# Kernel optimization log

Measured on AMD Instinct MI355X. Metric: run time of the kernel, lower is better.

Reference implementation:

```python
import jax, jax.numpy as jnp
import numpy as np

B, L, D = 4, 64, 512          # batch, trajectory length, d_model
DI, N, DC, R = 1024, 16, 4, 32  # d_inner, d_state, d_conv, dt_rank
NL = 4                         # n_layers
SD, AD, MEL = 17, 6, 1000      # state_dim, act_dim, max_ep_len
EPS = 1e-5


def setup_inputs() -> dict:
    key = jax.random.key(0)
    ks = iter(jax.random.split(key, 40))
    nrm = lambda shp, s=0.02: jax.random.normal(next(ks), shp, jnp.float32) * s
    inp = {
        "states": jax.random.normal(next(ks), (B, L, SD), jnp.float32),
        "actions": jax.random.normal(next(ks), (B, L, AD), jnp.float32),
        "returns_to_go": jax.random.normal(next(ks), (B, L, 1), jnp.float32),
        "constraints_to_go": jax.random.normal(next(ks), (B, L, 1), jnp.float32),
        "timesteps": jax.random.randint(next(ks), (B, L), 0, MEL, jnp.int32),
        # embedding / projection heads (torch Linear: y = x @ W.T + b)
        "es_w": nrm((D, SD)), "es_b": jnp.zeros((D,), jnp.float32),
        "ea_w": nrm((D, AD)), "ea_b": jnp.zeros((D,), jnp.float32),
        "er_w": nrm((D, 1)), "er_b": jnp.zeros((D,), jnp.float32),
        "ec_w": nrm((D, 1)), "ec_b": jnp.zeros((D,), jnp.float32),
        "et_w": nrm((MEL, D)),
        # per-layer Mamba params, stacked on leading NL axis
        "ln_w": jnp.ones((NL, D), jnp.float32), "ln_b": jnp.zeros((NL, D), jnp.float32),
        "in_w": nrm((NL, 2 * DI, D)),
        "conv_w": nrm((NL, DI, DC), 0.1), "conv_b": jnp.zeros((NL, DI), jnp.float32),
        "xp_w": nrm((NL, R + 2 * N, DI)),
        "dtp_w": nrm((NL, DI, R), 0.1),
        "dtp_b": jnp.full((NL, DI), -4.6, jnp.float32) + nrm((NL, DI), 0.1),
        "A_log": jnp.broadcast_to(jnp.log(jnp.arange(1, N + 1, dtype=jnp.float32)), (NL, DI, N)) * jnp.ones((NL, DI, 1), jnp.float32),
        "Dp": jnp.ones((NL, DI), jnp.float32),
        "out_w": nrm((NL, D, DI)),
        # final norm + heads
        "fn_w": jnp.ones((D,), jnp.float32), "fn_b": jnp.zeros((D,), jnp.float32),
        "ps_w": nrm((SD, D)), "ps_b": jnp.zeros((SD,), jnp.float32),
        "pa_w": nrm((AD, D)), "pa_b": jnp.zeros((AD,), jnp.float32),
    }
    return inp


def layernorm(x, w, b):
    mu = jnp.mean(x, -1, keepdims=True)
    var = jnp.mean(jnp.square(x - mu), -1, keepdims=True)
    return (x - mu) * jax.lax.rsqrt(var + EPS) * w + b


def selective_scan(u, delta, A, Bm, Cm, Dp):
    # u, delta: (B,T,DI); A: (DI,N); Bm, Cm: (B,T,N); Dp: (DI,)
    dA = jnp.exp(delta[..., None] * A)                      # (B,T,DI,N)
    dBu = delta[..., None] * Bm[:, :, None, :] * u[..., None]

    def step(h, xs):
        dA_t, dBu_t, C_t = xs
        h = dA_t * h + dBu_t                                # (B,DI,N)
        y = jnp.einsum('bdn,bn->bd', h, C_t)
        return h, y

    h0 = jnp.zeros((u.shape[0], u.shape[2], A.shape[1]), u.dtype)
    xs = (dA.transpose(1, 0, 2, 3), dBu.transpose(1, 0, 2, 3), Cm.transpose(1, 0, 2))
    _, ys = jax.lax.scan(step, h0, xs)
    return ys.transpose(1, 0, 2) + u * Dp


def mamba_mixer(x, in_w, conv_w, conv_b, xp_w, dtp_w, dtp_b, A_log, Dp, out_w):
    T = x.shape[1]
    xz = x @ in_w.T                                         # (B,T,2*DI)
    xm, z = jnp.split(xz, 2, axis=-1)
    # causal depthwise conv1d, kernel DC
    xpad = jnp.pad(xm, ((0, 0), (DC - 1, 0), (0, 0)))
    xc = sum(xpad[:, k:k + T, :] * conv_w[:, k] for k in range(DC)) + conv_b
    xc = jax.nn.silu(xc)
    dbc = xc @ xp_w.T                                       # (B,T,R+2N)
    dt, Bm, Cm = jnp.split(dbc, [R, R + N], axis=-1)
    delta = jax.nn.softplus(dt @ dtp_w.T + dtp_b)           # (B,T,DI)
    y = selective_scan(xc, delta, -jnp.exp(A_log), Bm, Cm, Dp)
    y = y * jax.nn.silu(z)
    return y @ out_w.T


def reference(states, actions, returns_to_go, constraints_to_go, timesteps,
              es_w, es_b, ea_w, ea_b, er_w, er_b, ec_w, ec_b, et_w,
              ln_w, ln_b, in_w, conv_w, conv_b, xp_w, dtp_w, dtp_b, A_log, Dp, out_w,
              fn_w, fn_b, ps_w, ps_b, pa_w, pa_b):
    te = et_w[timesteps]                                    # (B,L,D)
    se = states @ es_w.T + es_b + te
    ae = actions @ ea_w.T + ea_b + te
    re = returns_to_go @ er_w.T + er_b + te
    ce = constraints_to_go @ ec_w.T + ec_b + te
    # interleave (r, c, s, a) per timestep -> (B, 4L, D)
    x = jnp.stack((re, ce, se, ae), axis=2).reshape(B, 4 * L, D)
    for i in range(NL):
        x = x + mamba_mixer(layernorm(x, ln_w[i], ln_b[i]),
                            in_w[i], conv_w[i], conv_b[i], xp_w[i],
                            dtp_w[i], dtp_b[i], A_log[i], Dp[i], out_w[i])
    x = layernorm(x, fn_w, fn_b)
    outputs = x.reshape(B, L, 4, D).transpose(0, 2, 1, 3)   # (B,4,L,D)
    state_preds = outputs[:, 3] @ ps_w.T + ps_b             # from action tokens
    action_preds = outputs[:, 2] @ pa_w.T + pa_b            # from state tokens
    return state_preds, action_preds
```

## Files before the change

### kernel.cpp

```cpp
#include <hip/hip_runtime.h>
#include <math.h>

#define B_ 4
#define L_ 64
#define D_ 512
#define DI_ 1024
#define N_ 16
#define DC_ 4
#define R_ 32
#define NL_ 4
#define SD_ 17
#define AD_ 6
#define T_ 256
#define CH3_ 32
#define TC3_ 8
#define DL3_ 8

#define NW_IN  (NL_ * 2 * DI_ * D_)
#define NW_OUT (NL_ * D_ * DI_)
#define NW_XP  (NL_ * 64 * DI_)
#define NW_TOT (NW_IN + NW_OUT + NW_XP)

typedef short bf16x8 __attribute__((ext_vector_type(8)));
typedef float f32x4 __attribute__((ext_vector_type(4)));

__device__ __forceinline__ float silu_f(float v) { return v / (1.f + __expf(-v)); }
__device__ __forceinline__ float softplus_f(float v) {
    return fmaxf(v, 0.f) + log1pf(__expf(-fabsf(v)));
}
__device__ __forceinline__ unsigned short f2bs(float f) {
    unsigned u = __float_as_uint(f);
    u += 0x7fffu + ((u >> 16) & 1u);
    return (unsigned short)(u >> 16);
}
__device__ __forceinline__ float bs2f(unsigned short s) {
    return __uint_as_float(((unsigned)s) << 16);
}

__global__ __launch_bounds__(256) void wcvt_kernel(
    const float* __restrict__ in_w, const float* __restrict__ out_w,
    const float* __restrict__ xp_w, unsigned short* __restrict__ wb)
{
    const int i = blockIdx.x * 256 + threadIdx.x;
    if (i >= NW_TOT / 4) return;
    const int e = i * 4;
    const float* src; int off;
    if (e < NW_IN)               { src = in_w;  off = e; }
    else if (e < NW_IN + NW_OUT) { src = out_w; off = e - NW_IN; }
    else                         { src = xp_w;  off = e - NW_IN - NW_OUT; }
    const float4 v = *(const float4*)(src + off);
    ushort4 o;
    o.x = f2bs(v.x); o.y = f2bs(v.y); o.z = f2bs(v.z); o.w = f2bs(v.w);
    *(ushort4*)(wb + e) = o;
}

__global__ __launch_bounds__(512) void embed_kernel(
    const float* __restrict__ states, const float* __restrict__ actions,
    const float* __restrict__ rtg, const float* __restrict__ ctg,
    const int* __restrict__ ts,
    const float* __restrict__ es_w, const float* __restrict__ es_b,
    const float* __restrict__ ea_w, const float* __restrict__ ea_b,
    const float* __restrict__ er_w, const float* __restrict__ er_b,
    const float* __restrict__ ec_w, const float* __restrict__ ec_b,
    const float* __restrict__ et_w, float* __restrict__ x)
{
    const int bl = blockIdx.x;
    const int d = threadIdx.x;
    const float te = et_w[(size_t)ts[bl] * D_ + d];
    const float r = rtg[bl] * er_w[d] + er_b[d] + te;
    const float c = ctg[bl] * ec_w[d] + ec_b[d] + te;
    float s = es_b[d] + te;
#pragma unroll
    for (int k = 0; k < SD_; ++k) s += states[bl * SD_ + k] * es_w[d * SD_ + k];
    float a = ea_b[d] + te;
#pragma unroll
    for (int k = 0; k < AD_; ++k) a += actions[bl * AD_ + k] * ea_w[d * AD_ + k];
    float* xp = x + (size_t)bl * 4 * D_;
    xp[0 * D_ + d] = r;
    xp[1 * D_ + d] = c;
    xp[2 * D_ + d] = s;
    xp[3 * D_ + d] = a;
}

template <int MODE>
__global__ __launch_bounds__(256) void ln2_kernel(
    float* __restrict__ x, const float* __restrict__ p0,
    const float* __restrict__ p1,
    const float* __restrict__ w, const float* __restrict__ b,
    void* __restrict__ o_)
{
    const int tok = blockIdx.x;
    const int tid = threadIdx.x;
    float2 v = reinterpret_cast<float2*>(x + (size_t)tok * D_)[tid];
    if (MODE >= 1) {
        const float2 a0 = reinterpret_cast<const float2*>(p0 + (size_t)tok * D_)[tid];
        const float2 a1 = reinterpret_cast<const float2*>(p1 + (size_t)tok * D_)[tid];
        v.x += a0.x + a1.x;
        v.y += a0.y + a1.y;
        reinterpret_cast<float2*>(x + (size_t)tok * D_)[tid] = v;
    }
    float s = v.x + v.y;
#pragma unroll
    for (int off = 1; off < 64; off <<= 1) s += __shfl_xor(s, off);
    __shared__ float red[8];
    const int wv = tid >> 6;
    if ((tid & 63) == 0) red[wv] = s;
    __syncthreads();
    const float mean = (red[0] + red[1] + red[2] + red[3]) * (1.f / D_);
    const float dx = v.x - mean, dy = v.y - mean;
    float q = dx * dx + dy * dy;
#pragma unroll
    for (int off = 1; off < 64; off <<= 1) q += __shfl_xor(q, off);
    if ((tid & 63) == 0) red[4 + wv] = q;
    __syncthreads();
    const float var = (red[4] + red[5] + red[6] + red[7]) * (1.f / D_);
    const float r = rsqrtf(var + 1e-5f);
    const int d0 = tid * 2;
    const float o0 = dx * r * w[d0] + b[d0];
    const float o1 = dy * r * w[d0 + 1] + b[d0 + 1];
    if (MODE == 2) {
        float* o = (float*)o_;
        o[(size_t)tok * D_ + d0] = o0;
        o[(size_t)tok * D_ + d0 + 1] = o1;
    } else {
        unsigned short* o = (unsigned short*)o_;
        o[(size_t)tok * D_ + d0] = f2bs(o0);
        o[(size_t)tok * D_ + d0 + 1] = f2bs(o1);
    }
}

template <int MR, int NR, int EPI, int KT>
__global__ __launch_bounds__(256) void gemm3(
    const unsigned short* __restrict__ A, int lda,
    const unsigned short* __restrict__ W, int ldw,
    float* __restrict__ C, unsigned short* __restrict__ Cb1,
    unsigned short* __restrict__ Cb2, int N)
{
    const int lane = threadIdx.x & 63, wid = threadIdx.x >> 6;
    const int r = lane & 15, kq = lane >> 4;
    const int wm = blockIdx.y * (2 * MR * 16) + (wid >> 1) * (MR * 16);
    const int wn = blockIdx.x * (2 * NR * 16) + (wid & 1) * (NR * 16);
    const int kb = (EPI == 4) ? blockIdx.z * KT : 0;
    f32x4 acc[MR][NR] = {};
#pragma unroll 4
    for (int k0 = 0; k0 < KT; k0 += 32) {
        bf16x8 a[MR], b[NR];
#pragma unroll
        for (int i = 0; i < MR; ++i)
            a[i] = *(const bf16x8*)(A + (size_t)(wm + i * 16 + r) * lda + kb + k0 + kq * 8);
#pragma unroll
        for (int j = 0; j < NR; ++j)
            b[j] = *(const bf16x8*)(W + (size_t)(wn + j * 16 + r) * ldw + kb + k0 + kq * 8);
#pragma unroll
        for (int i = 0; i < MR; ++i)
#pragma unroll
            for (int j = 0; j < NR; ++j)
                acc[i][j] = __builtin_amdgcn_mfma_f32_16x16x32_bf16(a[i], b[j], acc[i][j], 0, 0, 0);
    }
#pragma unroll
    for (int i = 0; i < MR; ++i)
#pragma unroll
        for (int j = 0; j < NR; ++j)
#pragma unroll
            for (int g = 0; g < 4; ++g) {
                const int row = wm + i * 16 + kq * 4 + g;
                const int col = wn + j * 16 + r;
                const float val = acc[i][j][g];
                if (EPI == 3) {
                    if (col < DI_) Cb1[(size_t)row * DI_ + col] = f2bs(val);
                    else Cb2[(size_t)row * DI_ + (col - DI_)] = f2bs(silu_f(val));
                } else if (EPI == 4) {
                    C[(size_t)blockIdx.z * (1024 * 512) + (size_t)row * 512 + col] = val;
                } else {
                    C[(size_t)row * N + col] = val;
                }
            }
}

__global__ __launch_bounds__(256) void convxp_kernel(
    const unsigned short* __restrict__ xmb, const float* __restrict__ cw,
    const float* __restrict__ cb, const unsigned short* __restrict__ Wb,
    unsigned short* __restrict__ xcb, float* __restrict__ dbc)
{
    __shared__ unsigned short sA[16 * 1024];
    __shared__ float red[4][16][64];
    const int tid = threadIdx.x;
    const int m0 = blockIdx.x * 16;
    for (int task = tid; task < 16 * 128; task += 256) {
        const int rr = task >> 7;
        const int dd0 = (task & 127) * 8;
        const int row = m0 + rr;
        const int t = row & (T_ - 1);
        float4 cw4[8];
#pragma unroll
        for (int j = 0; j < 8; ++j) cw4[j] = ((const float4*)cw)[dd0 + j];
        float acc[8];
#pragma unroll
        for (int j = 0; j < 8; ++j) acc[j] = cb[dd0 + j];
#pragma unroll
        for (int k = 0; k < DC_; ++k) {
            if (t - 3 + k >= 0) {
                const bf16x8 v = *(const bf16x8*)(xmb + (size_t)(row - 3 + k) * DI_ + dd0);
#pragma unroll
                for (int j = 0; j < 8; ++j) {
                    const float wk = (k == 0) ? cw4[j].x : (k == 1) ? cw4[j].y
                                   : (k == 2) ? cw4[j].z : cw4[j].w;
                    acc[j] += wk * bs2f((unsigned short)v[j]);
                }
            }
        }
        bf16x8 ov;
#pragma unroll
        for (int j = 0; j < 8; ++j) ov[j] = (short)f2bs(silu_f(acc[j]));
        *(bf16x8*)(xcb + (size_t)row * DI_ + dd0) = ov;
        const int byteoff = (rr * 2048 + dd0 * 2) ^ ((rr & 7) << 4);
        *(bf16x8*)((char*)sA + byteoff) = ov;
    }
    __syncthreads();
    const int wid = tid >> 6, lane = tid & 63;
    const int r = lane & 15, kq = lane >> 4;
    f32x4 acc4[4] = {};
    const int k00 = wid * 256;
#pragma unroll
    for (int ks = 0; ks < 8; ++ks) {
        const int k0 = k00 + ks * 32;
        const int abyte = (r * 2048 + (k0 + kq * 8) * 2) ^ ((r & 7) << 4);
        const bf16x8 a = *(const bf16x8*)((const char*)sA + abyte);
#pragma unroll
        for (int j = 0; j < 4; ++j) {
            const bf16x8 bfr = *(const bf16x8*)(Wb + (size_t)(j * 16 + r) * DI_ + k0 + kq * 8);
            acc4[j] = __builtin_amdgcn_mfma_f32_16x16x32_bf16(a, bfr, acc4[j], 0, 0, 0);
        }
    }
#pragma unroll
    for (int j = 0; j < 4; ++j)
#pragma unroll
        for (int g = 0; g < 4; ++g)
            red[wid][kq * 4 + g][j * 16 + r] = acc4[j][g];
    __syncthreads();
    for (int i = tid; i < 1024; i += 256) {
        const int row = i >> 6, col = i & 63;
        const float s = red[0][row][col] + red[1][row][col] +
                        red[2][row][col] + red[3][row][col];
        dbc[(size_t)(m0 + row) * 64 + col] = s;
    }
}

__global__ __launch_bounds__(256, 3) void scan_kernel(
    const unsigned short* __restrict__ xcb, const float* __restrict__ dbc,
    const float* __restrict__ dtw, const float* __restrict__ dtbias,
    const float* __restrict__ A_log, const float* __restrict__ Dp,
    const unsigned short* __restrict__ zs, unsigned short* __restrict__ ygb)
{
    __shared__ float dlt_s[T_][DL3_ + 1];
    __shared__ float Sl[CH3_][DL3_][17];
    __shared__ float Pl[CH3_][DL3_][17];
    const int tid = threadIdx.x;
    const int dl = tid & (DL3_ - 1);
    const int c = tid >> 3;
    const int b = blockIdx.x >> 7;
    const int d = (blockIdx.x & 127) * DL3_ + dl;
    const int row0 = b * T_ + c * TC3_;
    {
        const float4* Wp = (const float4*)(dtw + (size_t)d * R_);
        float4 w4[8];
#pragma unroll
        for (int q = 0; q < 8; ++q) w4[q] = Wp[q];
        const float bias = dtbias[d];
#pragma unroll
        for (int t = 0; t < TC3_; ++t) {
            const float4* Ap = (const float4*)(dbc + (size_t)(row0 + t) * 64);
            float acc = bias;
#pragma unroll
            for (int q = 0; q < 8; ++q) {
                const float4 a4 = Ap[q];
                acc += a4.x * w4[q].x + a4.y * w4[q].y + a4.z * w4[q].z + a4.w * w4[q].w;
            }
            dlt_s[c * TC3_ + t][dl] = softplus_f(acc);
        }
    }
    float Av[N_];
    {
        const float4* Alp = (const float4*)(A_log + (size_t)d * N_);
#pragma unroll
        for (int q = 0; q < 4; ++q) {
            const float4 v = Alp[q];
            Av[q * 4 + 0] = -__expf(v.x);
            Av[q * 4 + 1] = -__expf(v.y);
            Av[q * 4 + 2] = -__expf(v.z);
            Av[q * 4 + 3] = -__expf(v.w);
        }
    }
    __syncthreads();
    const unsigned short* up = xcb + (size_t)row0 * DI_ + d;
    const float* bc = dbc + (size_t)row0 * 64;
    float h[N_];
#pragma unroll
    for (int n = 0; n < N_; ++n) h[n] = 0.f;
    float dsum = 0.f;
#pragma unroll
    for (int t = 0; t < TC3_; ++t) {
        const float dt_t = dlt_s[c * TC3_ + t][dl];
        dsum += dt_t;
        const float dbu = dt_t * bs2f(up[t * DI_]);
#pragma unroll
        for (int q = 0; q < 4; ++q) {
            const float4 b4 = *(const float4*)(bc + t * 64 + R_ + q * 4);
            h[q * 4 + 0] = __expf(dt_t * Av[q * 4 + 0]) * h[q * 4 + 0] + dbu * b4.x;
            h[q * 4 + 1] = __expf(dt_t * Av[q * 4 + 1]) * h[q * 4 + 1] + dbu * b4.y;
            h[q * 4 + 2] = __expf(dt_t * Av[q * 4 + 2]) * h[q * 4 + 2] + dbu * b4.z;
            h[q * 4 + 3] = __expf(dt_t * Av[q * 4 + 3]) * h[q * 4 + 3] + dbu * b4.w;
        }
    }
#pragma unroll
    for (int n = 0; n < N_; ++n) {
        Sl[c][dl][n] = h[n];
        Pl[c][dl][n] = __expf(Av[n] * dsum);
    }
    __syncthreads();
    if (tid < DL3_ * N_) {
        const int dd = tid >> 4, nn = tid & 15;
        float hin = 0.f;
#pragma unroll
        for (int c2 = 0; c2 < CH3_; ++c2) {
            const float t2 = Pl[c2][dd][nn] * hin + Sl[c2][dd][nn];
            Sl[c2][dd][nn] = hin;
            hin = t2;
        }
    }
    __syncthreads();
#pragma unroll
    for (int n = 0; n < N_; ++n) h[n] = Sl[c][dl][n];
    const float Dd = Dp[d];
    const unsigned short* zp = zs + (size_t)row0 * DI_ + d;
    unsigned short* yp = ygb + (size_t)row0 * DI_ + d;
#pragma unroll
    for (int t = 0; t < TC3_; ++t) {
        const float dt_t = dlt_s[c * TC3_ + t][dl];
        const float ut = bs2f(up[t * DI_]);
        const float dbu = dt_t * ut;
        float y = ut * Dd;
#pragma unroll
        for (int q = 0; q < 4; ++q) {
            const float4 b4 = *(const float4*)(bc + t * 64 + R_ + q * 4);
            const float4 c4 = *(const float4*)(bc + t * 64 + R_ + N_ + q * 4);
            h[q * 4 + 0] = __expf(dt_t * Av[q * 4 + 0]) * h[q * 4 + 0] + dbu * b4.x;
            h[q * 4 + 1] = __expf(dt_t * Av[q * 4 + 1]) * h[q * 4 + 1] + dbu * b4.y;
            h[q * 4 + 2] = __expf(dt_t * Av[q * 4 + 2]) * h[q * 4 + 2] + dbu * b4.z;
            h[q * 4 + 3] = __expf(dt_t * Av[q * 4 + 3]) * h[q * 4 + 3] + dbu * b4.w;
            y += h[q * 4 + 0] * c4.x + h[q * 4 + 1] * c4.y
               + h[q * 4 + 2] * c4.z + h[q * 4 + 3] * c4.w;
        }
        yp[t * DI_] = f2bs(y * bs2f(zp[t * DI_]));
    }
}

__global__ __launch_bounds__(256) void heads_kernel(
    const float* __restrict__ xn,
    const float* __restrict__ ps_w, const float* __restrict__ ps_b,
    const float* __restrict__ pa_w, const float* __restrict__ pa_b,
    float* __restrict__ out)
{
    const int idx = blockIdx.x * 4 + (threadIdx.x >> 6);
    const int lane = threadIdx.x & 63;
    const int bl = idx / 23, j = idx % 23;
    const float* tok;
    const float* wrow;
    float bias;
    float* dst;
    if (j < SD_) {
        tok = xn + ((size_t)bl * 4 + 3) * D_;
        wrow = ps_w + (size_t)j * D_;
        bias = ps_b[j];
        dst = out + (size_t)bl * SD_ + j;
    } else {
        const int jj = j - SD_;
        tok = xn + ((size_t)bl * 4 + 2) * D_;
        wrow = pa_w + (size_t)jj * D_;
        bias = pa_b[jj];
        dst = out + (size_t)B_ * L_ * SD_ + (size_t)bl * AD_ + jj;
    }
    float s = 0.f;
    for (int dd = lane; dd < D_; dd += 64) s += tok[dd] * wrow[dd];
#pragma unroll
    for (int off = 1; off < 64; off <<= 1) s += __shfl_xor(s, off);
    if (lane == 0) *dst = s + bias;
}

extern "C" void kernel_launch(void* const* d_in, const int* in_sizes, int n_in,
                              void* d_out, int out_size, void* d_ws, size_t ws_size,
                              hipStream_t stream)
{
    const float* states  = (const float*)d_in[0];
    const float* actions = (const float*)d_in[1];
    const float* rtg     = (const float*)d_in[2];
    const float* ctg     = (const float*)d_in[3];
    const int*   ts      = (const int*)d_in[4];
    const float* es_w = (const float*)d_in[5];  const float* es_b = (const float*)d_in[6];
    const float* ea_w = (const float*)d_in[7];  const float* ea_b = (const float*)d_in[8];
    const float* er_w = (const float*)d_in[9];  const float* er_b = (const float*)d_in[10];
    const float* ec_w = (const float*)d_in[11]; const float* ec_b = (const float*)d_in[12];
    const float* et_w = (const float*)d_in[13];
    const float* ln_w = (const float*)d_in[14]; const float* ln_b = (const float*)d_in[15];
    const float* in_w = (const float*)d_in[16];
    const float* conv_w = (const float*)d_in[17]; const float* conv_b = (const float*)d_in[18];
    const float* xp_w = (const float*)d_in[19];
    const float* dtp_w = (const float*)d_in[20]; const float* dtp_b = (const float*)d_in[21];
    const float* A_log = (const float*)d_in[22]; const float* Dp = (const float*)d_in[23];
    const float* out_w = (const float*)d_in[24];
    const float* fn_w = (const float*)d_in[25]; const float* fn_b = (const float*)d_in[26];
    const float* ps_w = (const float*)d_in[27]; const float* ps_b = (const float*)d_in[28];
    const float* pa_w = (const float*)d_in[29]; const float* pa_b = (const float*)d_in[30];
    float* out = (float*)d_out;

    float* ws   = (float*)d_ws;
    float* x    = ws;
    float* xn   = x + 524288;
    float* p    = xn + 524288;
    float* dbc  = p + 1048576;
    unsigned short* xnb = (unsigned short*)(dbc + 65536);
    unsigned short* xmb = xnb + 524288;
    unsigned short* xcb = xmb + 1048576;
    unsigned short* zs  = xcb + 1048576;
    unsigned short* ygb = zs + 1048576;
    unsigned short* wb  = ygb + 1048576;
    unsigned short* wb_in  = wb;
    unsigned short* wb_out = wb + NW_IN;
    unsigned short* wb_xp  = wb + NW_IN + NW_OUT;

    wcvt_kernel<<<(NW_TOT / 4 + 255) / 256, 256, 0, stream>>>(in_w, out_w, xp_w, wb);
    embed_kernel<<<B_ * L_, D_, 0, stream>>>(states, actions, rtg, ctg, ts,
        es_w, es_b, ea_w, ea_b, er_w, er_b, ec_w, ec_b, et_w, x);

    for (int i = 0; i < NL_; ++i) {
        if (i == 0)
            ln2_kernel<0><<<B_ * T_, 256, 0, stream>>>(
                x, nullptr, nullptr, ln_w, ln_b, xnb);
        else
            ln2_kernel<1><<<B_ * T_, 256, 0, stream>>>(
                x, p, p + 524288, ln_w + i * D_, ln_b + i * D_, xnb);
        gemm3<2, 2, 3, 512><<<dim3(32, 16), 256, 0, stream>>>(
            xnb, D_, wb_in + (size_t)i * 2 * DI_ * D_, D_, nullptr, xmb, zs, 2 * DI_);
        convxp_kernel<<<64, 256, 0, stream>>>(
            xmb, conv_w + i * DI_ * DC_, conv_b + i * DI_,
            wb_xp + (size_t)i * 64 * DI_, xcb, dbc);
        scan_kernel<<<B_ * (DI_ / DL3_), 256, 0, stream>>>(
            xcb, dbc, dtp_w + (size_t)i * DI_ * R_, dtp_b + i * DI_,
            A_log + (size_t)i * DI_ * N_, Dp + i * DI_, zs, ygb);
        gemm3<2, 2, 4, 512><<<dim3(8, 16, 2), 256, 0, stream>>>(
            ygb, DI_, wb_out + (size_t)i * D_ * DI_, DI_, p, nullptr, nullptr, D_);
    }

    ln2_kernel<2><<<B_ * T_, 256, 0, stream>>>(x, p, p + 524288, fn_w, fn_b, xn);
    heads_kernel<<<(B_ * L_ * 23) / 4, 256, 0, stream>>>(xn, ps_w, ps_b, pa_w, pa_b, out);
}
```

Before: 351.4 us.

## Increase grid parallelism: split conv/xproj over N, 4-way split-K out_proj, smaller in_proj tiles

The conv+x_proj kernel now launches a 2D grid that splits the 64 output columns across 4 blocks, so each block computes one 16-column MFMA tile and only the first column block writes the conv output. The out_proj GEMM moves to 4-way split-K with K chunks of 256 and smaller M tiles, and the in_proj GEMM uses half-height tiles with twice as many blocks. The layernorm kernel sums four partial buffers instead of two, which needs a larger workspace. The aim is to fill more CUs on this small problem, at the cost of recomputing the depthwise conv four times and adding extra partial-sum memory traffic.

```diff
diff --git a/kernel.cpp b/kernel.cpp
--- a/kernel.cpp
+++ b/kernel.cpp
@@ -84,8 +84,7 @@
 
 template <int MODE>
 __global__ __launch_bounds__(256) void ln2_kernel(
-    float* __restrict__ x, const float* __restrict__ p0,
-    const float* __restrict__ p1,
+    float* __restrict__ x, const float* __restrict__ p,
     const float* __restrict__ w, const float* __restrict__ b,
     void* __restrict__ o_)
 {
@@ -93,10 +92,12 @@
     const int tid = threadIdx.x;
     float2 v = reinterpret_cast<float2*>(x + (size_t)tok * D_)[tid];
     if (MODE >= 1) {
-        const float2 a0 = reinterpret_cast<const float2*>(p0 + (size_t)tok * D_)[tid];
-        const float2 a1 = reinterpret_cast<const float2*>(p1 + (size_t)tok * D_)[tid];
-        v.x += a0.x + a1.x;
-        v.y += a0.y + a1.y;
+#pragma unroll
+        for (int s4 = 0; s4 < 4; ++s4) {
+            const float2 a = reinterpret_cast<const float2*>(
+                p + (size_t)s4 * 524288 + (size_t)tok * D_)[tid];
+            v.x += a.x; v.y += a.y;
+        }
         reinterpret_cast<float2*>(x + (size_t)tok * D_)[tid] = v;
     }
     float s = v.x + v.y;
@@ -183,9 +184,10 @@
     unsigned short* __restrict__ xcb, float* __restrict__ dbc)
 {
     __shared__ unsigned short sA[16 * 1024];
-    __shared__ float red[4][16][64];
+    __shared__ float red[4][16][16];
     const int tid = threadIdx.x;
-    const int m0 = blockIdx.x * 16;
+    const int nq = blockIdx.x;
+    const int m0 = blockIdx.y * 16;
     for (int task = tid; task < 16 * 128; task += 256) {
         const int rr = task >> 7;
         const int dd0 = (task & 127) * 8;
@@ -212,37 +214,33 @@
         bf16x8 ov;
 #pragma unroll
         for (int j = 0; j < 8; ++j) ov[j] = (short)f2bs(silu_f(acc[j]));
-        *(bf16x8*)(xcb + (size_t)row * DI_ + dd0) = ov;
+        if (nq == 0)
+            *(bf16x8*)(xcb + (size_t)row * DI_ + dd0) = ov;
         const int byteoff = (rr * 2048 + dd0 * 2) ^ ((rr & 7) << 4);
         *(bf16x8*)((char*)sA + byteoff) = ov;
     }
     __syncthreads();
     const int wid = tid >> 6, lane = tid & 63;
     const int r = lane & 15, kq = lane >> 4;
-    f32x4 acc4[4] = {};
+    f32x4 acc4 = {};
     const int k00 = wid * 256;
 #pragma unroll
     for (int ks = 0; ks < 8; ++ks) {
         const int k0 = k00 + ks * 32;
         const int abyte = (r * 2048 + (k0 + kq * 8) * 2) ^ ((r & 7) << 4);
         const bf16x8 a = *(const bf16x8*)((const char*)sA + abyte);
-#pragma unroll
-        for (int j = 0; j < 4; ++j) {
-            const bf16x8 bfr = *(const bf16x8*)(Wb + (size_t)(j * 16 + r) * DI_ + k0 + kq * 8);
-            acc4[j] = __builtin_amdgcn_mfma_f32_16x16x32_bf16(a, bfr, acc4[j], 0, 0, 0);
-        }
-    }
-#pragma unroll
-    for (int j = 0; j < 4; ++j)
-#pragma unroll
-        for (int g = 0; g < 4; ++g)
-            red[wid][kq * 4 + g][j * 16 + r] = acc4[j][g];
-    __syncthreads();
-    for (int i = tid; i < 1024; i += 256) {
-        const int row = i >> 6, col = i & 63;
+        const bf16x8 bfr = *(const bf16x8*)(Wb + (size_t)(nq * 16 + r) * DI_ + k0 + kq * 8);
+        acc4 = __builtin_amdgcn_mfma_f32_16x16x32_bf16(a, bfr, acc4, 0, 0, 0);
+    }
+#pragma unroll
+    for (int g = 0; g < 4; ++g)
+        red[wid][kq * 4 + g][r] = acc4[g];
+    __syncthreads();
+    if (tid < 256) {
+        const int row = tid >> 4, col = tid & 15;
         const float s = red[0][row][col] + red[1][row][col] +
                         red[2][row][col] + red[3][row][col];
-        dbc[(size_t)(m0 + row) * 64 + col] = s;
+        dbc[(size_t)(m0 + row) * 64 + nq * 16 + col] = s;
     }
 }
 
@@ -417,7 +415,7 @@
     float* x    = ws;
     float* xn   = x + 524288;
     float* p    = xn + 524288;
-    float* dbc  = p + 1048576;
+    float* dbc  = p + 2097152;
     unsigned short* xnb = (unsigned short*)(dbc + 65536);
     unsigned short* xmb = xnb + 524288;
     unsigned short* xcb = xmb + 1048576;
@@ -435,22 +433,22 @@
     for (int i = 0; i < NL_; ++i) {
         if (i == 0)
             ln2_kernel<0><<<B_ * T_, 256, 0, stream>>>(
-                x, nullptr, nullptr, ln_w, ln_b, xnb);
+                x, nullptr, ln_w, ln_b, xnb);
         else
             ln2_kernel<1><<<B_ * T_, 256, 0, stream>>>(
-                x, p, p + 524288, ln_w + i * D_, ln_b + i * D_, xnb);
-        gemm3<2, 2, 3, 512><<<dim3(32, 16), 256, 0, stream>>>(
+                x, p, ln_w + i * D_, ln_b + i * D_, xnb);
+        gemm3<1, 2, 3, 512><<<dim3(32, 32), 256, 0, stream>>>(
             xnb, D_, wb_in + (size_t)i * 2 * DI_ * D_, D_, nullptr, xmb, zs, 2 * DI_);
-        convxp_kernel<<<64, 256, 0, stream>>>(
+        convxp_kernel<<<dim3(4, 64), 256, 0, stream>>>(
             xmb, conv_w + i * DI_ * DC_, conv_b + i * DI_,
             wb_xp + (size_t)i * 64 * DI_, xcb, dbc);
         scan_kernel<<<B_ * (DI_ / DL3_), 256, 0, stream>>>(
             xcb, dbc, dtp_w + (size_t)i * DI_ * R_, dtp_b + i * DI_,
             A_log + (size_t)i * DI_ * N_, Dp + i * DI_, zs, ygb);
-        gemm3<2, 2, 4, 512><<<dim3(8, 16, 2), 256, 0, stream>>>(
+        gemm3<1, 2, 4, 256><<<dim3(8, 32, 4), 256, 0, stream>>>(
             ygb, DI_, wb_out + (size_t)i * D_ * DI_, DI_, p, nullptr, nullptr, D_);
     }
 
-    ln2_kernel<2><<<B_ * T_, 256, 0, stream>>>(x, p, p + 524288, fn_w, fn_b, xn);
+    ln2_kernel<2><<<B_ * T_, 256, 0, stream>>>(x, p, fn_w, fn_b, xn);
     heads_kernel<<<(B_ * L_ * 23) / 4, 256, 0, stream>>>(xn, ps_w, ps_b, pa_w, pa_b, out);
 }
```

New measurement: 378.9 us. +7.8%, slower.
